# Performance work log

Measured on AMD Instinct MI355X. Metric: run time of the kernel, lower is better.

The kernel has to match this reference:

```python
import jax, jax.numpy as jnp
import numpy as np

IOU_THRES = 0.45
NEG_POS_RATIO = 3
BBOX_XFORM_CLIP = float(np.log(1000.0 / 16.0))  # torchvision BoxCoder clamp


def _make_boxes(key, shape, img=512.0):
    # valid xyxy boxes inside a 512x512 image
    k1, k2 = jax.random.split(key)
    cxy = jax.random.uniform(k1, shape + (2,), minval=32.0, maxval=img - 32.0)
    wh = jax.random.uniform(k2, shape + (2,), minval=8.0, maxval=128.0)
    return jnp.concatenate([cxy - 0.5 * wh, cxy + 0.5 * wh], axis=-1)


def setup_inputs() -> dict:
    key = jax.random.key(0)
    B, A, G, C = 32, 32768, 64, 91
    ks = jax.random.split(key, 5)
    return {
        "cls_logits": jax.random.normal(ks[0], (B, A, C), dtype=jnp.float32),
        "bbox_regression": 0.1 * jax.random.normal(ks[1], (B, A, 4), dtype=jnp.float32),
        "anchors": _make_boxes(ks[2], (B, A)),
        "gt_boxes": _make_boxes(ks[3], (B, G)),
        "gt_labels": jax.random.randint(ks[4], (B, G), 0, C - 1),  # fg classes; C-1 is background
    }


def _pairwise_iou(boxes, anchors):
    # boxes [B,G,4] xyxy, anchors [B,A,4] xyxy -> [B,G,A]
    b = boxes[:, :, None, :]
    a = anchors[:, None, :, :]
    tl = jnp.maximum(b[..., :2], a[..., :2])
    br = jnp.minimum(b[..., 2:], a[..., 2:])
    wh = jnp.clip(br - tl, 0.0)
    inter = wh[..., 0] * wh[..., 1]
    area_b = (b[..., 2] - b[..., 0]) * (b[..., 3] - b[..., 1])
    area_a = (a[..., 2] - a[..., 0]) * (a[..., 3] - a[..., 1])
    return inter / (area_b + area_a - inter + 1e-16)


def _match(ious):
    # SSDMatcher: per-anchor best gt, threshold, then force best anchor per gt.
    # ious [G,A] -> matches [A] in {-1, 0..G-1}
    G = ious.shape[0]
    vals = ious.max(axis=0)
    m = jnp.argmax(ious, axis=0)
    m = jnp.where(vals < IOU_THRES, -1, m)
    best_anchor_per_gt = jnp.argmax(ious, axis=1)  # [G]
    return m.at[best_anchor_per_gt].set(jnp.arange(G))


def _decode(reg, anchors):
    # torchvision BoxCoder.decode_single, weights (1,1,1,1), xyxy anchors
    w = anchors[..., 2] - anchors[..., 0]
    h = anchors[..., 3] - anchors[..., 1]
    cx = anchors[..., 0] + 0.5 * w
    cy = anchors[..., 1] + 0.5 * h
    dx, dy, dw, dh = reg[..., 0], reg[..., 1], reg[..., 2], reg[..., 3]
    dw = jnp.minimum(dw, BBOX_XFORM_CLIP)
    dh = jnp.minimum(dh, BBOX_XFORM_CLIP)
    pcx = dx * w + cx
    pcy = dy * h + cy
    pw = jnp.exp(dw) * w
    ph = jnp.exp(dh) * h
    return jnp.stack([pcx - 0.5 * pw, pcy - 0.5 * ph, pcx + 0.5 * pw, pcy + 0.5 * ph], axis=-1)


def _giou_loss(pred, gt):
    # GIoU loss on xyxy boxes; elementwise over leading dims
    tl = jnp.maximum(pred[..., :2], gt[..., :2])
    br = jnp.minimum(pred[..., 2:], gt[..., 2:])
    wh = jnp.clip(br - tl, 0.0)
    inter = wh[..., 0] * wh[..., 1]
    ap = (pred[..., 2] - pred[..., 0]) * (pred[..., 3] - pred[..., 1])
    ag = (gt[..., 2] - gt[..., 0]) * (gt[..., 3] - gt[..., 1])
    union = ap + ag - inter + 1e-16
    iou = inter / union
    ctl = jnp.minimum(pred[..., :2], gt[..., :2])
    cbr = jnp.maximum(pred[..., 2:], gt[..., 2:])
    cwh = cbr - ctl
    ac = cwh[..., 0] * cwh[..., 1]
    giou = iou - (ac - union) / jnp.clip(ac, 1e-16)
    return 1.0 - jnp.clip(giou, -1.0, 1.0)


def reference(cls_logits, bbox_regression, anchors, gt_boxes, gt_labels):
    B, A, C = cls_logits.shape
    # --- matching ---
    ious = _pairwise_iou(gt_boxes, anchors)        # [B,G,A]
    matched = jax.vmap(_match)(ious)               # [B,A]
    fg = matched >= 0                              # [B,A]
    idx = jnp.clip(matched, 0)
    num_fg = fg.sum()
    # --- bbox loss (sum over foreground only, via masking) ---
    matched_gt = jnp.take_along_axis(gt_boxes, idx[..., None], axis=1)  # [B,A,4]
    pred = _decode(bbox_regression, anchors)                            # [B,A,4]
    bbox_loss_sum = jnp.sum(_giou_loss(pred, matched_gt) * fg)
    # --- classification targets + CE ---
    matched_lbl = jnp.take_along_axis(gt_labels, idx, axis=1)           # [B,A]
    cls_targets = jnp.where(fg, matched_lbl, C - 1)
    logp = jax.nn.log_softmax(cls_logits, axis=-1)
    cls_loss = -jnp.take_along_axis(logp, cls_targets[..., None], axis=-1)[..., 0]  # [B,A]
    neg_loss = jnp.where(fg, -jnp.inf, cls_loss)
    order = jnp.argsort(-neg_loss, axis=1)         # descending
    rank = jnp.argsort(order, axis=1)
    num_neg = NEG_POS_RATIO * fg.sum(axis=1, keepdims=True)
    bg = rank < num_neg
    # --- normalize ---
    N = jnp.maximum(1, num_fg).astype(cls_loss.dtype)
    bbox_loss = 2.0 * bbox_loss_sum / N
    cls_total = (jnp.sum(cls_loss * fg) + jnp.sum(cls_loss * bg)) / N
    return jnp.stack([bbox_loss, cls_total])  # [bbox_loss, cls_loss]
```

## Files before the change

### kernel.cpp

```cpp
#include <hip/hip_runtime.h>
#include <hip/hip_bf16.h>

#define B 32
#define A 32768
#define G 64
#define C 91
#define NBINS 2048

typedef unsigned long long ull;

static constexpr size_t offMatched = 0;
static constexpr size_t offBits    = (size_t)B * A * 4;
static constexpr size_t offNumFg   = (size_t)2 * B * A * 4;
static constexpr size_t offAcc     = offNumFg + B * 4;
static constexpr size_t offTick    = offAcc + 3 * 8;
static constexpr size_t offGt      = offTick + 8;
static constexpr int    ZERO_N     = (int)((offGt - offNumFg) / 4);

__global__ void init_kernel(int* zero_base, ull* gtpack) {
  int i = blockIdx.x * 256 + threadIdx.x;
  if (i < ZERO_N) zero_base[i] = 0;
  if (i < B * G) gtpack[i] = 0xFFFFFFFFull;
}

__global__ __launch_bounds__(256) void match_kernel(
    const float4* __restrict__ anchors, const float4* __restrict__ gt_boxes,
    int* __restrict__ matched, ull* __restrict__ gtpack) {
#pragma clang fp contract(off)
  int b = blockIdx.y;
  int a = blockIdx.x * 256 + threadIdx.x;
  __shared__ float4 gtb[G];
  __shared__ float gtarea[G];
  __shared__ ull best[G];
  if (threadIdx.x < G) {
    float4 g = gt_boxes[b * G + threadIdx.x];
    gtb[threadIdx.x] = g;
    gtarea[threadIdx.x] = (g.z - g.x) * (g.w - g.y);
    best[threadIdx.x] = 0ull;
  }
  __syncthreads();
  float4 an = anchors[(size_t)b * A + a];
  float area_a = (an.z - an.x) * (an.w - an.y);
  float bestv = -1.0f;
  int bestg = 0;
  for (int g = 0; g < G; ++g) {
    float4 gb = gtb[g];
    float tlx = fmaxf(gb.x, an.x), tly = fmaxf(gb.y, an.y);
    float brx = fminf(gb.z, an.z), bry = fminf(gb.w, an.w);
    float w = fmaxf(brx - tlx, 0.0f), h = fmaxf(bry - tly, 0.0f);
    float inter = w * h;
    float iou = 0.0f;
    if (inter > 0.0f) iou = inter / (gtarea[g] + area_a - inter + 1e-16f);
    if (iou > bestv) { bestv = iou; bestg = g; }
    if (iou > 0.0f) {
      ull p = ((ull)__float_as_uint(iou) << 32) | (unsigned)(~(unsigned)a);
      if (p > best[g]) atomicMax(&best[g], p);
    }
  }
  matched[(size_t)b * A + a] = (bestv < 0.45f) ? -1 : bestg;
  __syncthreads();
  if (threadIdx.x < G) {
    ull p = best[threadIdx.x];
    if (p) atomicMax(&gtpack[b * G + threadIdx.x], p);
  }
}

__global__ void force_kernel(const ull* __restrict__ gtpack, int* __restrict__ matched) {
  int b = blockIdx.x * blockDim.x + threadIdx.x;
  if (b < B) {
    for (int g = 0; g < G; ++g) {
      unsigned a = ~(unsigned)(gtpack[b * G + g] & 0xFFFFFFFFull);
      matched[(size_t)b * A + a] = g;
    }
  }
}

#define APB 64
#define NT 8
#define NF4 (APB * C / 4)
#define NSTG 6
#define TAILN (NF4 - (NSTG - 1) * 256)

__device__ __forceinline__ void stage_tile(const float4* src, float* dst, int tid) {
  int wbase = tid & ~63;
#pragma unroll
  for (int r = 0; r < NSTG - 1; ++r)
    __builtin_amdgcn_global_load_lds(
        (const __attribute__((address_space(1))) void*)(src + r * 256 + tid),
        (__attribute__((address_space(3))) void*)(dst + (r * 256 + wbase) * 4),
        16, 0, 0);
  if (tid < TAILN)
    __builtin_amdgcn_global_load_lds(
        (const __attribute__((address_space(1))) void*)(src + (NSTG - 1) * 256 + tid),
        (__attribute__((address_space(3))) void*)(dst + ((NSTG - 1) * 256 + wbase) * 4),
        16, 0, 0);
}

__global__ __launch_bounds__(256) void loss_kernel(
    const float4* __restrict__ logit4, const float4* __restrict__ reg,
    const float4* __restrict__ anchors, const float4* __restrict__ gt_boxes,
    const int* __restrict__ gt_labels, const int* __restrict__ matched,
    unsigned* __restrict__ cls_bits, int* __restrict__ num_fg, double* __restrict__ acc) {
  __shared__ float buf[2][APB * C];
  __shared__ double rb[4], rf[4];
  __shared__ int rc[4];
  int tid = threadIdx.x;
  int b = blockIdx.y;
  int tile0 = blockIdx.x * NT;
  size_t bbase4 = (size_t)b * A * C / 4;
  int t4 = tid >> 2, q = tid & 3;

  stage_tile(logit4 + bbase4 + (size_t)tile0 * NF4, buf[0], tid);
  int mmCur = matched[(size_t)b * A + tile0 * APB + t4];
  int tclsCur = (mmCur >= 0) ? gt_labels[b * G + mmCur] : (C - 1);
  __syncthreads();

  double bbs = 0.0, fgs = 0.0;
  int cnt = 0;

  for (int t = 0; t < NT; ++t) {
    int cur = t & 1;
    if (t + 1 < NT)
      stage_tile(logit4 + bbase4 + (size_t)(tile0 + t + 1) * NF4, buf[cur ^ 1], tid);
    int mmNext = 0, tclsNext = 0;
    if (t + 1 < NT) {
      mmNext = matched[(size_t)b * A + (tile0 + t + 1) * APB + t4];
      tclsNext = (mmNext >= 0) ? gt_labels[b * G + mmNext] : (C - 1);
    }
    {
      const float* BC = buf[cur];
      int a = (tile0 + t) * APB + t4;
      const float* row = BC + t4 * C + 23 * q;
      const int cn = (q < 3) ? 23 : 22;
      float s0 = 0.f, s1 = 0.f, s2 = 0.f, s3 = 0.f;
      int j = 0;
#pragma unroll
      for (; j + 4 <= 20; j += 4) {
        s0 += __expf(row[j]);
        s1 += __expf(row[j + 1]);
        s2 += __expf(row[j + 2]);
        s3 += __expf(row[j + 3]);
      }
      for (; j < cn; ++j) s0 += __expf(row[j]);
      float s = (s0 + s1) + (s2 + s3);
      s += __shfl_xor(s, 1);
      s += __shfl_xor(s, 2);
      float lse = __logf(s);
      float xt = BC[t4 * C + tclsCur];
      float loss = lse - xt;
      if (q == 0) {
        cls_bits[(size_t)b * A + a] = (mmCur >= 0) ? 0u : __float_as_uint(loss);
        if (mmCur >= 0) {
          fgs += (double)loss;
          cnt++;
          float4 an = anchors[(size_t)b * A + a];
          float4 rg = reg[(size_t)b * A + a];
          float4 gb = gt_boxes[b * G + mmCur];
          float w = an.z - an.x, h = an.w - an.y;
          float cx = an.x + 0.5f * w, cy = an.y + 0.5f * h;
          float dw = fminf(rg.z, 4.135166556742356f);
          float dh = fminf(rg.w, 4.135166556742356f);
          float pcx = rg.x * w + cx, pcy = rg.y * h + cy;
          float pw = expf(dw) * w, ph = expf(dh) * h;
          float px0 = pcx - 0.5f * pw, py0 = pcy - 0.5f * ph;
          float px1 = pcx + 0.5f * pw, py1 = pcy + 0.5f * ph;
          float tlx = fmaxf(px0, gb.x), tly = fmaxf(py0, gb.y);
          float brx = fminf(px1, gb.z), bry = fminf(py1, gb.w);
          float iw = fmaxf(brx - tlx, 0.f), ih = fmaxf(bry - tly, 0.f);
          float inter = iw * ih;
          float ap = (px1 - px0) * (py1 - py0);
          float ag = (gb.z - gb.x) * (gb.w - gb.y);
          float uni = ap + ag - inter + 1e-16f;
          float iou = inter / uni;
          float ctlx = fminf(px0, gb.x), ctly = fminf(py0, gb.y);
          float cbrx = fmaxf(px1, gb.z), cbry = fmaxf(py1, gb.w);
          float acr = (cbrx - ctlx) * (cbry - ctly);
          float giou = iou - (acr - uni) / fmaxf(acr, 1e-16f);
          giou = fminf(fmaxf(giou, -1.f), 1.f);
          bbs += (double)(1.f - giou);
        }
      }
    }
    mmCur = mmNext;
    tclsCur = tclsNext;
    __syncthreads();
  }

  int lane = tid & 63, wave = tid >> 6;
  for (int off = 32; off; off >>= 1) {
    bbs += __shfl_xor(bbs, off);
    fgs += __shfl_xor(fgs, off);
    cnt += __shfl_xor(cnt, off);
  }
  if (lane == 0) { rb[wave] = bbs; rf[wave] = fgs; rc[wave] = cnt; }
  __syncthreads();
  if (tid == 0) {
    double tb = rb[0] + rb[1] + rb[2] + rb[3];
    double tf = rf[0] + rf[1] + rf[2] + rf[3];
    int tc = rc[0] + rc[1] + rc[2] + rc[3];
    if (tb != 0.0) atomicAdd(&acc[0], tb);
    if (tf != 0.0) atomicAdd(&acc[1], tf);
    if (tc) atomicAdd(&num_fg[b], tc);
  }
}

__global__ __launch_bounds__(1024) void select_fused(
    const unsigned* __restrict__ bits, const int* __restrict__ num_fg,
    double* __restrict__ acc, int* __restrict__ ticket, float* __restrict__ out) {
  int b = blockIdx.x, tid = threadIdx.x;
  __shared__ int h[NBINS];
  __shared__ int gsum[256];
  __shared__ float sT;
  __shared__ int sDone, sKrem, sR;
  __shared__ unsigned sPref;
  __shared__ double sd[16];

  unsigned bv[32];
#pragma unroll
  for (int i = 0; i < 32; ++i) bv[i] = bits[(size_t)b * A + i * 1024 + tid];
  if (tid == 0) { sDone = 0; sR = 0; }

  for (int i = tid; i < NBINS; i += 1024) h[i] = 0;
  __syncthreads();
#pragma unroll
  for (int i = 0; i < 32; ++i) atomicAdd(&h[bv[i] >> 21], 1);
  __syncthreads();
  if (tid < 256) {
    int gs = 0;
#pragma unroll
    for (int j = 0; j < 8; ++j) gs += h[tid * 8 + j];
    gsum[tid] = gs;
  }
  __syncthreads();
  if (tid == 0) {
    int nf = num_fg[b];
    int k = 3 * nf;
    int bgcnt = A - nf;
    if (k <= 0) { sT = __builtin_inff(); sDone = 1; }
    else if (k >= bgcnt) { sT = -1.0f; sDone = 1; }
    else {
      int run = 0, gidx = 255;
      for (; gidx >= 0; --gidx) { if (run + gsum[gidx] >= k) break; run += gsum[gidx]; }
      if (gidx < 0) { sT = -1.0f; sDone = 1; }
      else {
        int bin = gidx * 8 + 7;
        for (; bin > gidx * 8; --bin) { if (run + h[bin] >= k) break; run += h[bin]; }
        sPref = (unsigned)bin; sKrem = k - run;
      }
    }
  }
  __syncthreads();

  if (!sDone) {
    unsigned p1 = sPref;
    int k = sKrem;
    __syncthreads();
    for (int i = tid; i < NBINS; i += 1024) h[i] = 0;
    __syncthreads();
#pragma unroll
    for (int i = 0; i < 32; ++i)
      if ((bv[i] >> 21) == p1) atomicAdd(&h[(bv[i] >> 10) & 2047], 1);
    __syncthreads();
    if (tid < 256) {
      int gs = 0;
#pragma unroll
      for (int j = 0; j < 8; ++j) gs += h[tid * 8 + j];
      gsum[tid] = gs;
    }
    __syncthreads();
    if (tid == 0) {
      int run = 0, gidx = 255;
      for (; gidx >= 0; --gidx) { if (run + gsum[gidx] >= k) break; run += gsum[gidx]; }
      if (gidx < 0) { sT = -1.0f; sDone = 1; }
      else {
        int bin = gidx * 8 + 7;
        for (; bin > gidx * 8; --bin) { if (run + h[bin] >= k) break; run += h[bin]; }
        sPref = (p1 << 11) | (unsigned)bin; sKrem = k - run;
      }
    }
    __syncthreads();
  }
  if (!sDone) {
    unsigned p2 = sPref;
    int k = sKrem;
    __syncthreads();
    if (tid < 1024) h[tid] = 0;
    __syncthreads();
#pragma unroll
    for (int i = 0; i < 32; ++i)
      if ((bv[i] >> 10) == p2) atomicAdd(&h[bv[i] & 1023], 1);
    __syncthreads();
    if (tid < 256) {
      int gs = 0;
#pragma unroll
      for (int j = 0; j < 4; ++j) gs += h[tid * 4 + j];
      gsum[tid] = gs;
    }
    __syncthreads();
    if (tid == 0) {
      int run = 0, gidx = 255;
      for (; gidx >= 0; --gidx) { if (run + gsum[gidx] >= k) break; run += gsum[gidx]; }
      if (gidx < 0) { sT = -1.0f; }
      else {
        int bin = gidx * 4 + 3;
        for (; bin > gidx * 4; --bin) { if (run + h[bin] >= k) break; run += h[bin]; }
        sT = __uint_as_float((p2 << 10) | (unsigned)bin);
        sR = k - run;
      }
    }
    __syncthreads();
  }

  float T = sT;
  float ls = 0.f;
#pragma unroll
  for (int i = 0; i < 32; ++i) {
    float v = __uint_as_float(bv[i]);
    if (v > T) ls += v;
  }
  for (int off = 32; off; off >>= 1) ls += __shfl_xor(ls, off);
  if ((tid & 63) == 0) sd[tid >> 6] = (double)ls;
  __syncthreads();
  if (tid == 0) {
    double tt = 0.0;
    for (int w = 0; w < 16; ++w) tt += sd[w];
    if (sR > 0) tt += (double)sR * (double)sT;
    if (tt != 0.0) atomicAdd(&acc[2], tt);
    __threadfence();
    if (atomicAdd(ticket, 1) == B - 1) {
      int tot = 0;
      for (int bb = 0; bb < B; ++bb) tot += num_fg[bb];
      double N = (double)(tot > 1 ? tot : 1);
      double a2 = atomicAdd(&acc[2], 0.0);
      out[0] = (float)(2.0 * acc[0] / N);
      out[1] = (float)((acc[1] + a2) / N);
    }
  }
}

extern "C" void kernel_launch(void* const* d_in, const int* in_sizes, int n_in,
                              void* d_out, int out_size, void* d_ws, size_t ws_size,
                              hipStream_t stream) {
  const float4* logit4  = (const float4*)d_in[0];
  const float4* reg     = (const float4*)d_in[1];
  const float4* anchors = (const float4*)d_in[2];
  const float4* gtb     = (const float4*)d_in[3];
  const int*    gtl     = (const int*)d_in[4];

  char* ws = (char*)d_ws;
  int*      matched = (int*)(ws + offMatched);
  unsigned* cbits   = (unsigned*)(ws + offBits);
  int*      numfg   = (int*)(ws + offNumFg);
  double*   acc     = (double*)(ws + offAcc);
  int*      tick    = (int*)(ws + offTick);
  ull*      gtpack  = (ull*)(ws + offGt);
  float*    out     = (float*)d_out;

  init_kernel<<<8, 256, 0, stream>>>((int*)(ws + offNumFg), gtpack);
  match_kernel<<<dim3(A / 256, B), 256, 0, stream>>>(anchors, gtb, matched, gtpack);
  force_kernel<<<1, 64, 0, stream>>>(gtpack, matched);
  loss_kernel<<<dim3(A / (APB * NT), B), 256, 0, stream>>>(
      logit4, reg, anchors, gtb, gtl, matched, cbits, numfg, acc);
  select_fused<<<B, 1024, 0, stream>>>(cbits, numfg, acc, tick + 1, out);
}
```

Before: 713.3 us.

## Process four anchors per thread in matcher and halve loss tile size

```diff
diff --git a/kernel.cpp b/kernel.cpp
--- a/kernel.cpp
+++ b/kernel.cpp
@@ -23,12 +23,14 @@
   if (i < B * G) gtpack[i] = 0xFFFFFFFFull;
 }
 
+#define MAPB 1024
 __global__ __launch_bounds__(256) void match_kernel(
     const float4* __restrict__ anchors, const float4* __restrict__ gt_boxes,
     int* __restrict__ matched, ull* __restrict__ gtpack) {
 #pragma clang fp contract(off)
   int b = blockIdx.y;
-  int a = blockIdx.x * 256 + threadIdx.x;
+  int a0 = blockIdx.x * MAPB + threadIdx.x;
+  size_t abase = (size_t)b * A;
   __shared__ float4 gtb[G];
   __shared__ float gtarea[G];
   __shared__ ull best[G];
@@ -39,25 +41,39 @@
     best[threadIdx.x] = 0ull;
   }
   __syncthreads();
-  float4 an = anchors[(size_t)b * A + a];
-  float area_a = (an.z - an.x) * (an.w - an.y);
-  float bestv = -1.0f;
-  int bestg = 0;
+  float4 an[4];
+  float area_a[4];
+  float bestv[4];
+  int bestg[4];
+#pragma unroll
+  for (int k = 0; k < 4; ++k) {
+    an[k] = anchors[abase + a0 + k * 256];
+    area_a[k] = (an[k].z - an[k].x) * (an[k].w - an[k].y);
+    bestv[k] = -1.0f;
+    bestg[k] = 0;
+  }
   for (int g = 0; g < G; ++g) {
     float4 gb = gtb[g];
-    float tlx = fmaxf(gb.x, an.x), tly = fmaxf(gb.y, an.y);
-    float brx = fminf(gb.z, an.z), bry = fminf(gb.w, an.w);
-    float w = fmaxf(brx - tlx, 0.0f), h = fmaxf(bry - tly, 0.0f);
-    float inter = w * h;
-    float iou = 0.0f;
-    if (inter > 0.0f) iou = inter / (gtarea[g] + area_a - inter + 1e-16f);
-    if (iou > bestv) { bestv = iou; bestg = g; }
-    if (iou > 0.0f) {
-      ull p = ((ull)__float_as_uint(iou) << 32) | (unsigned)(~(unsigned)a);
-      if (p > best[g]) atomicMax(&best[g], p);
-    }
-  }
-  matched[(size_t)b * A + a] = (bestv < 0.45f) ? -1 : bestg;
+    float ga = gtarea[g];
+    ull pmax = 0ull;
+#pragma unroll
+    for (int k = 0; k < 4; ++k) {
+      float tlx = fmaxf(gb.x, an[k].x), tly = fmaxf(gb.y, an[k].y);
+      float brx = fminf(gb.z, an[k].z), bry = fminf(gb.w, an[k].w);
+      float w = fmaxf(brx - tlx, 0.0f), h = fmaxf(bry - tly, 0.0f);
+      float inter = w * h;
+      if (inter > 0.0f) {
+        float iou = inter / (ga + area_a[k] - inter + 1e-16f);
+        if (iou > bestv[k]) { bestv[k] = iou; bestg[k] = g; }
+        ull p = ((ull)__float_as_uint(iou) << 32) | (unsigned)(~(unsigned)(a0 + k * 256));
+        if (p > pmax) pmax = p;
+      }
+    }
+    if (pmax > best[g]) atomicMax(&best[g], pmax);
+  }
+#pragma unroll
+  for (int k = 0; k < 4; ++k)
+    matched[abase + a0 + k * 256] = (bestv[k] < 0.45f) ? -1 : bestg[k];
   __syncthreads();
   if (threadIdx.x < G) {
     ull p = best[threadIdx.x];
@@ -75,10 +91,10 @@
   }
 }
 
-#define APB 64
-#define NT 8
+#define APB 32
+#define NT 16
 #define NF4 (APB * C / 4)
-#define NSTG 6
+#define NSTG 3
 #define TAILN (NF4 - (NSTG - 1) * 256)
 
 __device__ __forceinline__ void stage_tile(const float4* src, float* dst, int tid) {
@@ -96,7 +112,7 @@
         16, 0, 0);
 }
 
-__global__ __launch_bounds__(256) void loss_kernel(
+__global__ __launch_bounds__(256, 6) void loss_kernel(
     const float4* __restrict__ logit4, const float4* __restrict__ reg,
     const float4* __restrict__ anchors, const float4* __restrict__ gt_boxes,
     const int* __restrict__ gt_labels, const int* __restrict__ matched,
@@ -108,10 +124,12 @@
   int b = blockIdx.y;
   int tile0 = blockIdx.x * NT;
   size_t bbase4 = (size_t)b * A * C / 4;
-  int t4 = tid >> 2, q = tid & 3;
+  int t8 = tid >> 3, q = tid & 7;
+  const int off = q * 11 + (q < 3 ? q : 3);
+  const int cn = 11 + (q < 3 ? 1 : 0);
 
   stage_tile(logit4 + bbase4 + (size_t)tile0 * NF4, buf[0], tid);
-  int mmCur = matched[(size_t)b * A + tile0 * APB + t4];
+  int mmCur = matched[(size_t)b * A + tile0 * APB + t8];
   int tclsCur = (mmCur >= 0) ? gt_labels[b * G + mmCur] : (C - 1);
   __syncthreads();
 
@@ -124,29 +142,28 @@
       stage_tile(logit4 + bbase4 + (size_t)(tile0 + t + 1) * NF4, buf[cur ^ 1], tid);
     int mmNext = 0, tclsNext = 0;
     if (t + 1 < NT) {
-      mmNext = matched[(size_t)b * A + (tile0 + t + 1) * APB + t4];
+      mmNext = matched[(size_t)b * A + (tile0 + t + 1) * APB + t8];
       tclsNext = (mmNext >= 0) ? gt_labels[b * G + mmNext] : (C - 1);
     }
     {
       const float* BC = buf[cur];
-      int a = (tile0 + t) * APB + t4;
-      const float* row = BC + t4 * C + 23 * q;
-      const int cn = (q < 3) ? 23 : 22;
+      int a = (tile0 + t) * APB + t8;
+      const float* row = BC + t8 * C + off;
       float s0 = 0.f, s1 = 0.f, s2 = 0.f, s3 = 0.f;
-      int j = 0;
-#pragma unroll
-      for (; j + 4 <= 20; j += 4) {
+#pragma unroll
+      for (int j = 0; j < 8; j += 4) {
         s0 += __expf(row[j]);
         s1 += __expf(row[j + 1]);
         s2 += __expf(row[j + 2]);
         s3 += __expf(row[j + 3]);
       }
-      for (; j < cn; ++j) s0 += __expf(row[j]);
+      for (int j = 8; j < cn; ++j) s0 += __expf(row[j]);
       float s = (s0 + s1) + (s2 + s3);
       s += __shfl_xor(s, 1);
       s += __shfl_xor(s, 2);
+      s += __shfl_xor(s, 4);
       float lse = __logf(s);
-      float xt = BC[t4 * C + tclsCur];
+      float xt = BC[t8 * C + tclsCur];
       float loss = lse - xt;
       if (q == 0) {
         cls_bits[(size_t)b * A + a] = (mmCur >= 0) ? 0u : __float_as_uint(loss);
@@ -187,10 +204,10 @@
   }
 
   int lane = tid & 63, wave = tid >> 6;
-  for (int off = 32; off; off >>= 1) {
-    bbs += __shfl_xor(bbs, off);
-    fgs += __shfl_xor(fgs, off);
-    cnt += __shfl_xor(cnt, off);
+  for (int o = 32; o; o >>= 1) {
+    bbs += __shfl_xor(bbs, o);
+    fgs += __shfl_xor(fgs, o);
+    cnt += __shfl_xor(cnt, o);
   }
   if (lane == 0) { rb[wave] = bbs; rf[wave] = fgs; rc[wave] = cnt; }
   __syncthreads();
@@ -318,7 +335,7 @@
     float v = __uint_as_float(bv[i]);
     if (v > T) ls += v;
   }
-  for (int off = 32; off; off >>= 1) ls += __shfl_xor(ls, off);
+  for (int o = 32; o; o >>= 1) ls += __shfl_xor(ls, o);
   if ((tid & 63) == 0) sd[tid >> 6] = (double)ls;
   __syncthreads();
   if (tid == 0) {
@@ -357,7 +374,7 @@
   float*    out     = (float*)d_out;
 
   init_kernel<<<8, 256, 0, stream>>>((int*)(ws + offNumFg), gtpack);
-  match_kernel<<<dim3(A / 256, B), 256, 0, stream>>>(anchors, gtb, matched, gtpack);
+  match_kernel<<<dim3(A / MAPB, B), 256, 0, stream>>>(anchors, gtb, matched, gtpack);
   force_kernel<<<1, 64, 0, stream>>>(gtpack, matched);
   loss_kernel<<<dim3(A / (APB * NT), B), 256, 0, stream>>>(
       logit4, reg, anchors, gtb, gtl, matched, cbits, numfg, acc);
```

New measurement: 758.6 us. 6.3% more time.

## Prefetch match indices upfront and pipeline logit staging two tiles ahead

Applied to the files above, without the earlier changes.

```diff
diff --git a/kernel.cpp b/kernel.cpp
--- a/kernel.cpp
+++ b/kernel.cpp
@@ -110,25 +110,30 @@
   size_t bbase4 = (size_t)b * A * C / 4;
   int t4 = tid >> 2, q = tid & 3;
 
+  int mm[NT], tcls[NT];
+#pragma unroll
+  for (int t = 0; t < NT; ++t) {
+    mm[t] = matched[(size_t)b * A + (tile0 + t) * APB + t4];
+    tcls[t] = (mm[t] >= 0) ? gt_labels[b * G + mm[t]] : (C - 1);
+  }
+
   stage_tile(logit4 + bbase4 + (size_t)tile0 * NF4, buf[0], tid);
-  int mmCur = matched[(size_t)b * A + tile0 * APB + t4];
-  int tclsCur = (mmCur >= 0) ? gt_labels[b * G + mmCur] : (C - 1);
-  __syncthreads();
+  stage_tile(logit4 + bbase4 + (size_t)(tile0 + 1) * NF4, buf[1], tid);
 
   double bbs = 0.0, fgs = 0.0;
   int cnt = 0;
 
+#pragma unroll
   for (int t = 0; t < NT; ++t) {
-    int cur = t & 1;
-    if (t + 1 < NT)
-      stage_tile(logit4 + bbase4 + (size_t)(tile0 + t + 1) * NF4, buf[cur ^ 1], tid);
-    int mmNext = 0, tclsNext = 0;
-    if (t + 1 < NT) {
-      mmNext = matched[(size_t)b * A + (tile0 + t + 1) * APB + t4];
-      tclsNext = (mmNext >= 0) ? gt_labels[b * G + mmNext] : (C - 1);
-    }
+    if (t < NT - 1) {
+      asm volatile("s_waitcnt vmcnt(5)" ::: "memory");
+    } else {
+      asm volatile("s_waitcnt vmcnt(0)" ::: "memory");
+    }
+    __builtin_amdgcn_s_barrier();
+    __builtin_amdgcn_sched_barrier(0);
     {
-      const float* BC = buf[cur];
+      const float* BC = buf[t & 1];
       int a = (tile0 + t) * APB + t4;
       const float* row = BC + t4 * C + 23 * q;
       const int cn = (q < 3) ? 23 : 22;
@@ -146,16 +151,16 @@
       s += __shfl_xor(s, 1);
       s += __shfl_xor(s, 2);
       float lse = __logf(s);
-      float xt = BC[t4 * C + tclsCur];
+      float xt = BC[t4 * C + tcls[t]];
       float loss = lse - xt;
       if (q == 0) {
-        cls_bits[(size_t)b * A + a] = (mmCur >= 0) ? 0u : __float_as_uint(loss);
-        if (mmCur >= 0) {
+        cls_bits[(size_t)b * A + a] = (mm[t] >= 0) ? 0u : __float_as_uint(loss);
+        if (mm[t] >= 0) {
           fgs += (double)loss;
           cnt++;
           float4 an = anchors[(size_t)b * A + a];
           float4 rg = reg[(size_t)b * A + a];
-          float4 gb = gt_boxes[b * G + mmCur];
+          float4 gb = gt_boxes[b * G + mm[t]];
           float w = an.z - an.x, h = an.w - an.y;
           float cx = an.x + 0.5f * w, cy = an.y + 0.5f * h;
           float dw = fminf(rg.z, 4.135166556742356f);
@@ -181,16 +186,17 @@
         }
       }
     }
-    mmCur = mmNext;
-    tclsCur = tclsNext;
-    __syncthreads();
+    __builtin_amdgcn_s_barrier();
+    __builtin_amdgcn_sched_barrier(0);
+    if (t + 2 < NT)
+      stage_tile(logit4 + bbase4 + (size_t)(tile0 + t + 2) * NF4, buf[t & 1], tid);
   }
 
   int lane = tid & 63, wave = tid >> 6;
-  for (int off = 32; off; off >>= 1) {
-    bbs += __shfl_xor(bbs, off);
-    fgs += __shfl_xor(fgs, off);
-    cnt += __shfl_xor(cnt, off);
+  for (int o = 32; o; o >>= 1) {
+    bbs += __shfl_xor(bbs, o);
+    fgs += __shfl_xor(fgs, o);
+    cnt += __shfl_xor(cnt, o);
   }
   if (lane == 0) { rb[wave] = bbs; rf[wave] = fgs; rc[wave] = cnt; }
   __syncthreads();
@@ -318,7 +324,7 @@
     float v = __uint_as_float(bv[i]);
     if (v > T) ls += v;
   }
-  for (int off = 32; off; off >>= 1) ls += __shfl_xor(ls, off);
+  for (int o = 32; o; o >>= 1) ls += __shfl_xor(ls, o);
   if ((tid & 63) == 0) sd[tid >> 6] = (double)ls;
   __syncthreads();
   if (tid == 0) {
```

New measurement: 710.6 us. No clear change (-0.4%).
